# Performance work log

Measured on AMD Instinct MI355X. Metric: run time of the kernel, lower is better.

## Reference

```python
import jax, jax.numpy as jnp
import numpy as np

HEADS = 16

def setup_inputs() -> dict:
    key = jax.random.key(0)
    ks = jax.random.split(key, 5)
    B, N, C = 2, 2048, 1024
    s = 0.02
    return {
        "x": jax.random.normal(ks[0], (B, N, C), jnp.float32),
        "y": jax.random.normal(ks[1], (B, N, C), jnp.float32),
        "w_qkv": jax.random.normal(ks[2], (C, 3 * C), jnp.float32) * s,  # acts as Linear weight^T
        "w_proj": jax.random.normal(ks[3], (C, C), jnp.float32) * s,
        "b_proj": jnp.zeros((C,), jnp.float32),
    }

def _qkv_heads(t, w_qkv, B, N, H, D):
    qkv = (t @ w_qkv).reshape(B, N, 3, H, D)
    qkv = jnp.transpose(qkv, (2, 0, 3, 1, 4))  # [3, B, H, N, D]
    return qkv[0], qkv[1], qkv[2]

def reference(x, y, w_qkv, w_proj, b_proj):
    B, N, C = x.shape
    H = HEADS
    D = C // H
    scale = D ** (-0.5)
    q, k, v = _qkv_heads(x, w_qkv, B, N, H, D)
    q1, k1, v1 = _qkv_heads(y, w_qkv, B, N, H, D)
    attn = jax.nn.softmax(jnp.einsum('bhnd,bhmd->bhnm', q, k) * scale, axis=-1)
    attn1 = jax.nn.softmax(jnp.einsum('bhnd,bhmd->bhnm', q1, k1) * scale, axis=-1)
    # cross-swapped values: x-branch attends over v1 (from y), y-branch over v (from x)
    ox = jnp.einsum('bhnm,bhmd->bhnd', attn, v1)
    oy = jnp.einsum('bhnm,bhmd->bhnd', attn1, v)
    ox = jnp.transpose(ox, (0, 2, 1, 3)).reshape(B, N, C)
    oy = jnp.transpose(oy, (0, 2, 1, 3)).reshape(B, N, C)
    x_out = ox @ w_proj + b_proj + x
    y_out = oy @ w_proj + b_proj + y
    return x_out, y_out
```

## Files before the change

### kernel.cpp

```cpp
#include <hip/hip_runtime.h>

using u16    = unsigned short;
using short8 = __attribute__((ext_vector_type(8))) short;
using f32x4  = __attribute__((ext_vector_type(4))) float;
using f32x16 = __attribute__((ext_vector_type(16))) float;

#define MFMA16(a, b, c) __builtin_amdgcn_mfma_f32_16x16x32_bf16(a, b, c, 0, 0, 0)
#define MFMA32(a, b, c) __builtin_amdgcn_mfma_f32_32x32x16_bf16(a, b, c, 0, 0, 0)

#define QSCALE 0.18033688011112042f

__device__ inline u16 f2bf(float f) {
  union { float f; unsigned u; } v; v.f = f;
  unsigned r = v.u + 0x7fffu + ((v.u >> 16) & 1u);
  return (u16)(r >> 16);
}

__device__ __forceinline__ void load_lds16(const u16* g, u16* l) {
  __builtin_amdgcn_global_load_lds((const __attribute__((address_space(1))) void*)g,
                                   (__attribute__((address_space(3))) void*)l, 16, 0, 0);
}

__device__ __forceinline__ unsigned cvt_pk_bf16(float lo, float hi) {
  unsigned r;
  asm("v_cvt_pk_bf16_f32 %0, %1, %2" : "=v"(r) : "v"(lo), "v"(hi));
  return r;
}

__device__ __forceinline__ void plswap(unsigned& a, unsigned& b) {
  auto r = __builtin_amdgcn_permlane32_swap(a, b, false, false);
  a = r[0];
  b = r[1];
}

__global__ __launch_bounds__(256) void cvt_k(const float* __restrict__ src,
                                             u16* __restrict__ dst) {
  const int i = (blockIdx.x * 256 + threadIdx.x) * 8;
  const float4 a = *(const float4*)&src[i];
  const float4 b = *(const float4*)&src[i + 4];
  short8 o;
  o[0] = (short)f2bf(a.x); o[1] = (short)f2bf(a.y);
  o[2] = (short)f2bf(a.z); o[3] = (short)f2bf(a.w);
  o[4] = (short)f2bf(b.x); o[5] = (short)f2bf(b.y);
  o[6] = (short)f2bf(b.z); o[7] = (short)f2bf(b.w);
  *(short8*)&dst[i] = o;
}

__global__ __launch_bounds__(256) void cvtT_k(const float* __restrict__ src,
                                              u16* __restrict__ dst, int R, int C) {
  __shared__ float t[64][65];
  const int c0 = blockIdx.x * 64, r0 = blockIdx.y * 64;
  const int lc = threadIdx.x & 63, g = threadIdx.x >> 6;
#pragma unroll
  for (int i = 0; i < 16; ++i) {
    const int r = g + i * 4;
    t[r][lc] = src[(size_t)(r0 + r) * C + c0 + lc];
  }
  __syncthreads();
#pragma unroll
  for (int i = 0; i < 16; ++i) {
    const int c = g + i * 4;
    dst[(size_t)(c0 + c) * R + r0 + lc] = f2bf(t[lc][c]);
  }
}

template <int MODE>
__global__ __launch_bounds__(256, 2) void gemm_k(
    const u16* __restrict__ A0, const u16* __restrict__ A1,
    const u16* __restrict__ Bt,
    u16* __restrict__ q_out, u16* __restrict__ k_out, u16* __restrict__ v_out,
    float* __restrict__ c0, float* __restrict__ c1,
    const float* __restrict__ bias,
    const float* __restrict__ res0, const float* __restrict__ res1) {
  __shared__ alignas(16) u16 lA[128 * 64];
  __shared__ alignas(16) u16 lB[128 * 64];
  const int z = blockIdx.z;
  const u16* A = z ? A1 : A0;
  float* c_out = z ? c1 : c0;
  const float* res = z ? res1 : res0;
  const int head_base = z * 32;

  const int tid = threadIdx.x;
  const int lane = tid & 63, wave = tid >> 6;
  const int quad = lane >> 4, l16 = lane & 15;
  const int lsw = (l16 & 7) * 8;
  const int wm = (wave >> 1) * 64, wn = (wave & 1) * 64;
  const int bn0 = blockIdx.x * 128, bm0 = blockIdx.y * 128;
  const int srow = lane >> 3;
  const int sg = (lane & 7) ^ srow;

  f32x4 acc[4][4] = {};

  for (int k0 = 0; k0 < 1024; k0 += 64) {
    __syncthreads();
#pragma unroll
    for (int it = 0; it < 4; ++it) {
      const int rb = wave * 32 + it * 8;
      const int r = rb + srow;
      load_lds16(&A[(size_t)(bm0 + r) * 1024 + k0 + sg * 8], &lA[rb * 64]);
      load_lds16(&Bt[(size_t)(bn0 + r) * 1024 + k0 + sg * 8], &lB[rb * 64]);
    }
    asm volatile("s_waitcnt vmcnt(0)" ::: "memory");
    __syncthreads();
#pragma unroll
    for (int kt = 0; kt < 2; ++kt) {
      short8 af[4], bfr[4];
#pragma unroll
      for (int i = 0; i < 4; ++i) {
        const int go = ((kt * 4 + quad) * 8) ^ lsw;
        af[i]  = *(const short8*)&lA[(wm + i * 16 + l16) * 64 + go];
        bfr[i] = *(const short8*)&lB[(wn + i * 16 + l16) * 64 + go];
      }
#pragma unroll
      for (int i = 0; i < 4; ++i)
#pragma unroll
        for (int j = 0; j < 4; ++j)
          acc[i][j] = MFMA16(af[i], bfr[j], acc[i][j]);
    }
  }

#pragma unroll
  for (int i = 0; i < 4; ++i) {
    const int row = bm0 + wm + i * 16 + quad * 4;
#pragma unroll
    for (int j = 0; j < 4; ++j) {
      const int col = bn0 + wn + j * 16 + l16;
#pragma unroll
      for (int r = 0; r < 4; ++r) {
        const float v = acc[i][j][r];
        const int m = row + r;
        if (MODE == 0) {
          const int which = col >> 10;
          const int h = (col >> 6) & 15, d = col & 63;
          const int b = m >> 11, n = m & 2047;
          const size_t hh = (size_t)(head_base + b * 16 + h);
          if (which == 0)      q_out[(hh * 2048 + n) * 64 + d] = f2bf(v * QSCALE);
          else if (which == 1) k_out[(hh * 2048 + n) * 64 + d] = f2bf(v);
          else                 v_out[(hh * 64 + d) * 2048 + n] = f2bf(v);
        } else {
          const size_t idx = (size_t)m * 1024 + col;
          c_out[idx] = v + bias[col] + res[idx];
        }
      }
    }
  }
}

__global__ __launch_bounds__(256, 4) void attn_k(const u16* __restrict__ Q,
                                                 const u16* __restrict__ K,
                                                 const u16* __restrict__ V,
                                                 u16* __restrict__ O) {
  __shared__ alignas(16) u16 kT[64 * 64];
  __shared__ alignas(16) u16 vT[64 * 64];

  const int tid = threadIdx.x;
  const int lane = tid & 63, wave = tid >> 6;
  const int qn = lane & 31, h = lane >> 5;
  const int s = blockIdx.z >> 1, b = blockIdx.z & 1, hh = blockIdx.y;
  const int head_qk = (s * 2 + b) * 16 + hh;
  const int head_v  = ((1 - s) * 2 + b) * 16 + hh;
  const u16* Qh = Q + (size_t)head_qk * 2048 * 64;
  const u16* Kh = K + (size_t)head_qk * 2048 * 64;
  const u16* Vh = V + (size_t)head_v * 64 * 2048;
  const int qr0 = blockIdx.x * 128 + wave * 32;

  short8 qf[4];
#pragma unroll
  for (int f = 0; f < 4; ++f)
    qf[f] = *(const short8*)&Qh[(size_t)(qr0 + qn) * 64 + f * 16 + h * 8];

  f32x16 oacc[2] = {};
  float l_i = 0.f;

  const int srow = lane >> 3;

  union PU { unsigned u[4]; short8 s; };

  for (int j0 = 0; j0 < 2048; j0 += 64) {
    __syncthreads();
#pragma unroll
    for (int it = 0; it < 2; ++it) {
      const int rb = wave * 16 + it * 8;
      const int r = rb + srow;
      const int sgx = (lane & 7) ^ srow ^ (rb >> 3);
      load_lds16(&Kh[(size_t)(j0 + r) * 64 + sgx * 8], &kT[rb * 64]);
      load_lds16(&Vh[(size_t)r * 2048 + j0 + sgx * 8], &vT[rb * 64]);
    }
    asm volatile("s_waitcnt vmcnt(0)" ::: "memory");
    __syncthreads();

    f32x16 sacc[2] = {};
#pragma unroll
    for (int t = 0; t < 2; ++t) {
      const int row = t * 32 + qn;
      const int key = (row & 7) ^ (row >> 3);
#pragma unroll
      for (int kd = 0; kd < 4; ++kd) {
        const int go = ((kd * 2 + h) ^ key) * 8;
        const short8 kf = *(const short8*)&kT[row * 64 + go];
        sacc[t] = MFMA32(kf, qf[kd], sacc[t]);
      }
    }

    float rs = 0.f;
    unsigned pw[2][8];
#pragma unroll
    for (int t = 0; t < 2; ++t)
#pragma unroll
      for (int j = 0; j < 8; ++j) {
        const float pa0 = exp2f(sacc[t][2 * j]);
        const float pa1 = exp2f(sacc[t][2 * j + 1]);
        rs += pa0 + pa1;
        pw[t][j] = cvt_pk_bf16(pa0, pa1);
      }

    PU pa[4];
#pragma unroll
    for (int t = 0; t < 2; ++t)
#pragma unroll
      for (int e = 0; e < 2; ++e) {
        unsigned a0 = pw[t][4 * e + 0], a2 = pw[t][4 * e + 2];
        unsigned a1 = pw[t][4 * e + 1], a3 = pw[t][4 * e + 3];
        plswap(a0, a2);
        plswap(a1, a3);
        pa[2 * t + e].u[0] = a0; pa[2 * t + e].u[1] = a1;
        pa[2 * t + e].u[2] = a2; pa[2 * t + e].u[3] = a3;
      }

    rs += __shfl_xor(rs, 32, 64);
    l_i += rs;

#pragma unroll
    for (int dt = 0; dt < 2; ++dt) {
      const int row = dt * 32 + qn;
      const int key = (row & 7) ^ (row >> 3);
#pragma unroll
      for (int st = 0; st < 4; ++st) {
        const int go = ((st * 2 + h) ^ key) * 8;
        const short8 vf = *(const short8*)&vT[row * 64 + go];
        oacc[dt] = MFMA32(pa[st].s, vf, oacc[dt]);
      }
    }
  }

  u16* Ob = O + (size_t)s * 4096 * 1024;
#pragma unroll
  for (int r = 0; r < 16; ++r) {
    const int qrow = (r & 3) + 8 * (r >> 2) + 4 * h;
    const float lr = __shfl(l_i, qrow, 64);
    const float inv = 1.f / lr;
    const size_t base = (size_t)(b * 2048 + qr0 + qrow) * 1024 + hh * 64;
#pragma unroll
    for (int dt = 0; dt < 2; ++dt)
      Ob[base + dt * 32 + qn] = f2bf(oacc[dt][r] * inv);
  }
}

extern "C" void kernel_launch(void* const* d_in, const int* in_sizes, int n_in,
                              void* d_out, int out_size, void* d_ws, size_t ws_size,
                              hipStream_t stream) {
  const float* x      = (const float*)d_in[0];
  const float* y      = (const float*)d_in[1];
  const float* w_qkv  = (const float*)d_in[2];
  const float* w_proj = (const float*)d_in[3];
  const float* b_proj = (const float*)d_in[4];
  float* out = (float*)d_out;

  u16* xb     = (u16*)d_ws;
  u16* yb     = xb + 4194304;
  u16* Ob     = xb;
  u16* wqkvT  = yb + 4194304;
  u16* wprojT = wqkvT + 3145728;
  u16* Qs     = wprojT + 1048576;
  u16* Ks     = Qs + 8388608;
  u16* Vs     = Ks + 8388608;

  cvt_k<<<2048, 256, 0, stream>>>(x, xb);
  cvt_k<<<2048, 256, 0, stream>>>(y, yb);
  cvtT_k<<<dim3(48, 16), 256, 0, stream>>>(w_qkv, wqkvT, 1024, 3072);
  cvtT_k<<<dim3(16, 16), 256, 0, stream>>>(w_proj, wprojT, 1024, 1024);

  gemm_k<0><<<dim3(24, 32, 2), 256, 0, stream>>>(xb, yb, wqkvT, Qs, Ks, Vs,
                                                 nullptr, nullptr, nullptr,
                                                 nullptr, nullptr);

  attn_k<<<dim3(16, 16, 4), 256, 0, stream>>>(Qs, Ks, Vs, Ob);

  gemm_k<1><<<dim3(8, 32, 2), 256, 0, stream>>>(Ob, Ob + 4194304, wprojT,
                                                nullptr, nullptr, nullptr,
                                                out, out + 4194304, b_proj, x, y);
}
```

Measured before the change: 327.9 us.

## Double-buffer K/V tiles in attention, swizzle block order, use native exp2

The attention kernel now keeps two LDS buffers for K and V, so the next 64-key tile is fetched while the current one is computed, with one barrier per iteration instead of two. The grid becomes 1D and block indices are remapped so that blocks sharing the same K/V head are spread across the XCD round-robin pattern to improve L2 locality. exp2f is replaced with the hardware exp2 builtin. LDS use doubles (32KB per block), which may limit occupancy at the 4-blocks-per-CU launch bound.

```diff
diff --git a/kernel.cpp b/kernel.cpp
--- a/kernel.cpp
+++ b/kernel.cpp
@@ -150,19 +150,26 @@
                                                  const u16* __restrict__ K,
                                                  const u16* __restrict__ V,
                                                  u16* __restrict__ O) {
-  __shared__ alignas(16) u16 kT[64 * 64];
-  __shared__ alignas(16) u16 vT[64 * 64];
+  __shared__ alignas(16) u16 kT[2][64 * 64];
+  __shared__ alignas(16) u16 vT[2][64 * 64];
 
   const int tid = threadIdx.x;
   const int lane = tid & 63, wave = tid >> 6;
   const int qn = lane & 31, h = lane >> 5;
-  const int s = blockIdx.z >> 1, b = blockIdx.z & 1, hh = blockIdx.y;
-  const int head_qk = (s * 2 + b) * 16 + hh;
-  const int head_v  = ((1 - s) * 2 + b) * 16 + hh;
+
+  const int d0 = blockIdx.x;
+  const int swz = ((d0 & 7) << 7) | (d0 >> 3);
+  const int qx = swz & 15;
+  const int hh = (swz >> 4) & 15;
+  const int z  = swz >> 8;
+  const int s = z >> 1, b = z & 1;
+
+  const int head_qk = z * 16 + hh;
+  const int head_v  = (z ^ 2) * 16 + hh;
   const u16* Qh = Q + (size_t)head_qk * 2048 * 64;
   const u16* Kh = K + (size_t)head_qk * 2048 * 64;
   const u16* Vh = V + (size_t)head_v * 64 * 2048;
-  const int qr0 = blockIdx.x * 128 + wave * 32;
+  const int qr0 = qx * 128 + wave * 32;
 
   short8 qf[4];
 #pragma unroll
@@ -176,18 +183,26 @@
 
   union PU { unsigned u[4]; short8 s; };
 
-  for (int j0 = 0; j0 < 2048; j0 += 64) {
-    __syncthreads();
+  auto stage = [&](int buf, int j0) {
 #pragma unroll
     for (int it = 0; it < 2; ++it) {
       const int rb = wave * 16 + it * 8;
       const int r = rb + srow;
       const int sgx = (lane & 7) ^ srow ^ (rb >> 3);
-      load_lds16(&Kh[(size_t)(j0 + r) * 64 + sgx * 8], &kT[rb * 64]);
-      load_lds16(&Vh[(size_t)r * 2048 + j0 + sgx * 8], &vT[rb * 64]);
-    }
-    asm volatile("s_waitcnt vmcnt(0)" ::: "memory");
-    __syncthreads();
+      load_lds16(&Kh[(size_t)(j0 + r) * 64 + sgx * 8], &kT[buf][rb * 64]);
+      load_lds16(&Vh[(size_t)r * 2048 + j0 + sgx * 8], &vT[buf][rb * 64]);
+    }
+  };
+
+  stage(0, 0);
+  asm volatile("s_waitcnt vmcnt(0)" ::: "memory");
+  __syncthreads();
+
+  int cur = 0;
+  for (int j0 = 0; j0 < 2048; j0 += 64) {
+    if (j0 + 64 < 2048) stage(cur ^ 1, j0 + 64);
+    const u16* kb = kT[cur];
+    const u16* vb = vT[cur];
 
     f32x16 sacc[2] = {};
 #pragma unroll
@@ -197,7 +212,7 @@
 #pragma unroll
       for (int kd = 0; kd < 4; ++kd) {
         const int go = ((kd * 2 + h) ^ key) * 8;
-        const short8 kf = *(const short8*)&kT[row * 64 + go];
+        const short8 kf = *(const short8*)&kb[row * 64 + go];
         sacc[t] = MFMA32(kf, qf[kd], sacc[t]);
       }
     }
@@ -208,8 +223,8 @@
     for (int t = 0; t < 2; ++t)
 #pragma unroll
       for (int j = 0; j < 8; ++j) {
-        const float pa0 = exp2f(sacc[t][2 * j]);
-        const float pa1 = exp2f(sacc[t][2 * j + 1]);
+        const float pa0 = __builtin_amdgcn_exp2f(sacc[t][2 * j]);
+        const float pa1 = __builtin_amdgcn_exp2f(sacc[t][2 * j + 1]);
         rs += pa0 + pa1;
         pw[t][j] = cvt_pk_bf16(pa0, pa1);
       }
@@ -237,10 +252,14 @@
 #pragma unroll
       for (int st = 0; st < 4; ++st) {
         const int go = ((st * 2 + h) ^ key) * 8;
-        const short8 vf = *(const short8*)&vT[row * 64 + go];
+        const short8 vf = *(const short8*)&vb[row * 64 + go];
         oacc[dt] = MFMA32(pa[st].s, vf, oacc[dt]);
       }
     }
+
+    asm volatile("s_waitcnt vmcnt(0)" ::: "memory");
+    __syncthreads();
+    cur ^= 1;
   }
 
   u16* Ob = O + (size_t)s * 4096 * 1024;
@@ -284,7 +303,7 @@
                                                  nullptr, nullptr, nullptr,
                                                  nullptr, nullptr);
 
-  attn_k<<<dim3(16, 16, 4), 256, 0, stream>>>(Qs, Ks, Vs, Ob);
+  attn_k<<<1024, 256, 0, stream>>>(Qs, Ks, Vs, Ob);
 
   gemm_k<1><<<dim3(8, 32, 2), 256, 0, stream>>>(Ob, Ob + 4194304, wprojT,
                                                 nullptr, nullptr, nullptr,
```

After: 296.2 us. 9.7% less time.
